# Performance work log

Hardware: AMD Instinct MI355X
Metric: run time of the kernel (lower is better)

## Reference

```python
import jax, jax.numpy as jnp
import numpy as np

E = 16      # num_experts
K = 4       # num_experts_per_tok
H = 2048    # hidden_size
I = 1408    # moe_intermediate_size
SI = 5632   # shared expert intermediate size
CAP = 1024
NORM_TOPK = False


def setup_inputs() -> dict:
    key = jax.random.key(0)
    ks = jax.random.split(key, 9)
    def w(k, shape, fan_in):
        return jax.random.normal(k, shape, jnp.float32) * (fan_in ** -0.5)
    return {
        "hidden_states": jax.random.normal(ks[0], (1, 2048, H), jnp.float32),
        "gate_w":  w(ks[1], (E, H), H),        # router: Linear(H -> E), no bias
        "we_gate": w(ks[2], (E, I, H), H),     # per-expert gate_proj weights
        "we_up":   w(ks[3], (E, I, H), H),     # per-expert up_proj weights
        "we_down": w(ks[4], (E, H, I), I),     # per-expert down_proj weights
        "ws_gate": w(ks[5], (SI, H), H),       # shared expert gate_proj
        "ws_up":   w(ks[6], (SI, H), H),       # shared expert up_proj
        "ws_down": w(ks[7], (H, SI), SI),      # shared expert down_proj
        "sg_w":    w(ks[8], (1, H), H),        # shared_expert_gate: Linear(H -> 1)
    }


def reference(hidden_states, gate_w, we_gate, we_up, we_down,
              ws_gate, ws_up, ws_down, sg_w):
    B, S, Hd = hidden_states.shape
    x = hidden_states.reshape(-1, Hd)                      # [T, H]
    T = x.shape[0]

    # --- router ---
    router_logits = x @ gate_w.T                           # [T, E]
    probs = jax.nn.softmax(router_logits.astype(jnp.float32), axis=-1)
    topw, topi = jax.lax.top_k(probs, K)                   # [T, K]
    if NORM_TOPK:
        topw = topw / topw.sum(axis=-1, keepdims=True)

    # --- dispatch: flatten (token, slot) assignments ---
    A = T * K
    fe = topi.reshape(A)                                   # expert id per assignment
    fw = topw.reshape(A)                                   # routing weight per assignment
    ft = jnp.repeat(jnp.arange(T), K)                      # token id per assignment
    # position of each assignment within its expert (rank in arrival order)
    oh = jax.nn.one_hot(fe, E, dtype=jnp.int32)            # [A, E]
    pos = jnp.take_along_axis(jnp.cumsum(oh, axis=0) - 1, fe[:, None], axis=1)[:, 0]
    valid = pos < CAP
    # scatter tokens into per-expert buffers; overflow goes to dummy row CAP
    buf = jnp.zeros((E, CAP + 1, Hd), x.dtype)
    buf = buf.at[fe, jnp.where(valid, pos, CAP)].set(x[ft])[:, :CAP]  # [E, C, H]

    # --- per-expert SiLU-gated MLP (batched grouped GEMMs) ---
    g = jnp.einsum('ech,eih->eci', buf, we_gate)
    u = jnp.einsum('ech,eih->eci', buf, we_up)
    eo = jnp.einsum('eci,ehi->ech', jax.nn.silu(g) * u, we_down)      # [E, C, H]

    # --- combine: weighted scatter-add back to tokens ---
    ga = eo[fe, jnp.minimum(pos, CAP - 1)]                 # [A, H]
    wcomb = (fw * valid.astype(fw.dtype)).astype(x.dtype)
    y = jnp.zeros((T, Hd), x.dtype).at[ft].add(ga * wcomb[:, None])

    # --- shared expert with sigmoid gate ---
    sh = (jax.nn.silu(x @ ws_gate.T) * (x @ ws_up.T)) @ ws_down.T
    sh = jax.nn.sigmoid(x @ sg_w.T) * sh

    out = (y + sh).reshape(B, S, Hd)
    return out, router_logits
```

## Files before the change

kernel.cpp:

```cpp
#include <hip/hip_runtime.h>

#define T_TOK 2048
#define NE 16
#define KTOP 4
#define HD 2048
#define ID 1408
#define SID 5632
#define CAPACITY 1024

typedef __attribute__((ext_vector_type(8))) short short8;
typedef __attribute__((ext_vector_type(4))) float floatx4;

__device__ __forceinline__ short f2b(float f){
  union { float f; unsigned u; } v; v.f = f;
  unsigned r = v.u + 0x7fffu + ((v.u >> 16) & 1u);
  return (short)(r >> 16);
}

__device__ __forceinline__ void gl16(const void* g, void* l){
  __builtin_amdgcn_global_load_lds(
      (const __attribute__((address_space(1))) void*)g,
      (__attribute__((address_space(3))) void*)l, 16, 0, 0);
}

__global__ void moe_zero(int* __restrict__ counts){
  if (threadIdx.x < NE) counts[threadIdx.x] = 0;
}

__global__ void moe_convert(const float* __restrict__ src, short* __restrict__ dst, int n8){
  int stride = gridDim.x * blockDim.x;
  for (int i = blockIdx.x * blockDim.x + threadIdx.x; i < n8; i += stride){
    float4 f0 = ((const float4*)src)[(size_t)i * 2];
    float4 f1 = ((const float4*)src)[(size_t)i * 2 + 1];
    short8 v = { f2b(f0.x), f2b(f0.y), f2b(f0.z), f2b(f0.w),
                 f2b(f1.x), f2b(f1.y), f2b(f1.z), f2b(f1.w) };
    ((short8*)dst)[i] = v;
  }
}

__global__ void moe_router(const float* __restrict__ x,
                           const float* __restrict__ gate_w,
                           const float* __restrict__ sg_w,
                           float* __restrict__ logits_out,
                           short* __restrict__ xb,
                           int* __restrict__ counts,
                           int* __restrict__ slot_token,
                           float* __restrict__ slot_w,
                           float* __restrict__ sg)
{
  int wave = threadIdx.x >> 6, lane = threadIdx.x & 63;
  int t = (blockIdx.x << 2) + wave;
  if (t >= T_TOK) return;
  const float4* xr = (const float4*)(x + (size_t)t * HD);
  short8* xbw = (short8*)(xb + (size_t)t * HD);
  float acc[17];
  #pragma unroll
  for (int e = 0; e < 17; ++e) acc[e] = 0.f;
  #pragma unroll
  for (int j = 0; j < 4; ++j){
    int i4 = (j * 64 + lane) * 2;
    float4 x0 = xr[i4], x1 = xr[i4 + 1];
    short8 v = { f2b(x0.x), f2b(x0.y), f2b(x0.z), f2b(x0.w),
                 f2b(x1.x), f2b(x1.y), f2b(x1.z), f2b(x1.w) };
    xbw[j * 64 + lane] = v;
    #pragma unroll
    for (int e = 0; e < 16; ++e){
      const float4* gr = (const float4*)(gate_w + e * HD);
      float4 g0 = gr[i4], g1 = gr[i4 + 1];
      acc[e] += x0.x*g0.x + x0.y*g0.y + x0.z*g0.z + x0.w*g0.w
              + x1.x*g1.x + x1.y*g1.y + x1.z*g1.z + x1.w*g1.w;
    }
    const float4* sr = (const float4*)sg_w;
    float4 s0 = sr[i4], s1 = sr[i4 + 1];
    acc[16] += x0.x*s0.x + x0.y*s0.y + x0.z*s0.z + x0.w*s0.w
             + x1.x*s1.x + x1.y*s1.y + x1.z*s1.z + x1.w*s1.w;
  }
  #pragma unroll
  for (int e = 0; e < 17; ++e){
    float v = acc[e];
    #pragma unroll
    for (int off = 32; off > 0; off >>= 1) v += __shfl_xor(v, off, 64);
    acc[e] = v;
  }
  if (lane == 0){
    float m = acc[0];
    #pragma unroll
    for (int e = 1; e < 16; ++e) m = fmaxf(m, acc[e]);
    float p[16]; float s = 0.f;
    #pragma unroll
    for (int e = 0; e < 16; ++e){ p[e] = expf(acc[e] - m); s += p[e]; }
    float inv = 1.f / s;
    #pragma unroll
    for (int e = 0; e < 16; ++e) logits_out[t * 16 + e] = acc[e];
    unsigned used = 0;
    for (int k = 0; k < KTOP; ++k){
      float best = -1.f; int bi = 0;
      #pragma unroll
      for (int e = 0; e < 16; ++e){
        float pe = ((used >> e) & 1u) ? -1.f : p[e];
        if (pe > best){ best = pe; bi = e; }
      }
      used |= (1u << bi);
      int pos = atomicAdd(&counts[bi], 1);
      if (pos < CAPACITY){
        slot_token[bi * CAPACITY + pos] = t;
        slot_w[bi * CAPACITY + pos] = best * inv;
      }
    }
    sg[t] = 1.f / (1.f + expf(-acc[16]));
  }
}


template<int BF16W>
__global__ __launch_bounds__(256) void moe_gateup(
    const short* __restrict__ Asrc,
    const void* __restrict__ Wg_, const void* __restrict__ Wu_,
    short* __restrict__ Out,
    const int* __restrict__ counts, const int* __restrict__ slot_token,
    int Ndim, int Kdim, int expert_mode, int mtiles, int ntiles)
{
  int nwg = gridDim.x;
  int wg = ((blockIdx.x & 7) * (nwg >> 3)) + (blockIdx.x >> 3);
  int m_t = wg % mtiles; wg /= mtiles;
  int n_t = wg % ntiles; int e = wg / ntiles;

  int cnt = T_TOK;
  size_t woff = 0;
  short* out = Out;
  if (expert_mode){
    cnt = counts[e]; if (cnt > CAPACITY) cnt = CAPACITY;
    if (m_t * 128 >= cnt) return;
    woff = (size_t)e * Ndim * Kdim;
    out = Out + (size_t)e * CAPACITY * Ndim;
  }
  const int m0 = m_t * 128, n0 = n_t * 64;

  __shared__ __align__(16) char smem[32768];
  char* sA  = smem;
  char* sBg = smem + 16384;
  char* sBu = smem + 24576;

  const int tid = threadIdx.x;
  const int lane = tid & 63, wave = tid >> 6;
  const int wr = wave >> 1, wc = wave & 1;
  const int lrow = lane & 15, lk = lane >> 4;

  const int srow  = tid >> 3;
  const int sxor  = srow & 7;
  const int pslot = tid & 7;
  const int lslot = pslot ^ sxor;

  const short* aptr[4];
  #pragma unroll
  for (int i = 0; i < 4; ++i){
    int p = m0 + i * 32 + srow;
    const short* base;
    if (expert_mode){
      int q = (p < cnt) ? p : 0;
      base = Asrc + (size_t)slot_token[e * CAPACITY + q] * Kdim;
    } else {
      base = Asrc + (size_t)p * Kdim;
    }
    aptr[i] = base + (lslot << 3);
  }
  const short *bgp[2], *bup[2];
  const float *bgf[2], *buf2[2];
  #pragma unroll
  for (int i = 0; i < 2; ++i){
    size_t roff = (size_t)(n0 + i * 32 + srow) * Kdim + (lslot << 3);
    if (BF16W){
      bgp[i] = (const short*)Wg_ + woff + roff;
      bup[i] = (const short*)Wu_ + woff + roff;
    } else {
      bgf[i]  = (const float*)Wg_ + woff + roff;
      buf2[i] = (const float*)Wu_ + woff + roff;
    }
  }

  const floatx4 vzero = {0.f, 0.f, 0.f, 0.f};
  floatx4 accg[4][2], accu[4][2];
  #pragma unroll
  for (int i = 0; i < 4; ++i)
    #pragma unroll
    for (int j = 0; j < 2; ++j){ accg[i][j] = vzero; accu[i][j] = vzero; }

  const int fxor = lrow & 7;
  const int arowb = (wr * 64 + lrow) << 7;
  const int browb = (wc * 32 + lrow) << 7;

  for (int k0 = 0; k0 < Kdim; k0 += 64){
    __syncthreads();
    if (BF16W){
      #pragma unroll
      for (int i = 0; i < 4; ++i) gl16(aptr[i] + k0, sA  + i * 4096 + tid * 16);
      #pragma unroll
      for (int i = 0; i < 2; ++i) gl16(bgp[i] + k0, sBg + i * 4096 + tid * 16);
      #pragma unroll
      for (int i = 0; i < 2; ++i) gl16(bup[i] + k0, sBu + i * 4096 + tid * 16);
    } else {
      #pragma unroll
      for (int i = 0; i < 4; ++i){
        short8 v = *(const short8*)(aptr[i] + k0);
        *(short8*)(sA + i * 4096 + tid * 16) = v;
      }
      #pragma unroll
      for (int i = 0; i < 2; ++i){
        float4 f0 = *(const float4*)(bgf[i] + k0);
        float4 f1 = *(const float4*)(bgf[i] + k0 + 4);
        short8 v = { f2b(f0.x), f2b(f0.y), f2b(f0.z), f2b(f0.w),
                     f2b(f1.x), f2b(f1.y), f2b(f1.z), f2b(f1.w) };
        *(short8*)(sBg + i * 4096 + tid * 16) = v;
        float4 g0 = *(const float4*)(buf2[i] + k0);
        float4 g1 = *(const float4*)(buf2[i] + k0 + 4);
        short8 w = { f2b(g0.x), f2b(g0.y), f2b(g0.z), f2b(g0.w),
                     f2b(g1.x), f2b(g1.y), f2b(g1.z), f2b(g1.w) };
        *(short8*)(sBu + i * 4096 + tid * 16) = w;
      }
    }
    __syncthreads();
    #pragma unroll
    for (int kh = 0; kh < 2; ++kh){
      const int soff = (((kh << 2) | lk) ^ fxor) << 4;
      short8 a[4], bg[2], bu[2];
      #pragma unroll
      for (int mf = 0; mf < 4; ++mf)
        a[mf] = *(const short8*)(sA + arowb + (mf << 11) + soff);
      #pragma unroll
      for (int nf = 0; nf < 2; ++nf){
        bg[nf] = *(const short8*)(sBg + browb + (nf << 11) + soff);
        bu[nf] = *(const short8*)(sBu + browb + (nf << 11) + soff);
      }
      #pragma unroll
      for (int mf = 0; mf < 4; ++mf)
        #pragma unroll
        for (int nf = 0; nf < 2; ++nf){
          accg[mf][nf] = __builtin_amdgcn_mfma_f32_16x16x32_bf16(a[mf], bg[nf], accg[mf][nf], 0, 0, 0);
          accu[mf][nf] = __builtin_amdgcn_mfma_f32_16x16x32_bf16(a[mf], bu[nf], accu[mf][nf], 0, 0, 0);
        }
    }
  }

  const int colbase = n0 + wc * 32 + lrow;
  #pragma unroll
  for (int mf = 0; mf < 4; ++mf){
    int pr = m0 + wr * 64 + mf * 16 + lk * 4;
    #pragma unroll
    for (int nf = 0; nf < 2; ++nf){
      floatx4 g4 = accg[mf][nf], u4 = accu[mf][nf];
      int col = colbase + nf * 16;
      #pragma unroll
      for (int r = 0; r < 4; ++r){
        float gv = g4[r], uv = u4[r];
        float a = (gv / (1.f + __expf(-gv))) * uv;
        out[(size_t)(pr + r) * Ndim + col] = f2b(a);
      }
    }
  }
}

template<int BF16W>
__global__ __launch_bounds__(256) void moe_down(
    const short* __restrict__ Asrc,
    const void* __restrict__ Wd_,
    float* __restrict__ y,
    const int* __restrict__ counts, const int* __restrict__ slot_token,
    const float* __restrict__ slot_w, const float* __restrict__ sgate,
    int Kdim, int expert_mode, int mtiles, int ntiles)
{
  int nwg = gridDim.x;
  int wg = ((blockIdx.x & 7) * (nwg >> 3)) + (blockIdx.x >> 3);
  int m_t = wg % mtiles; wg /= mtiles;
  int n_t = wg % ntiles; int e = wg / ntiles;

  int cnt = T_TOK;
  const short* ab = Asrc;
  size_t woff = 0;
  if (expert_mode){
    cnt = counts[e]; if (cnt > CAPACITY) cnt = CAPACITY;
    if (m_t * 128 >= cnt) return;
    ab = Asrc + (size_t)e * CAPACITY * Kdim;
    woff = (size_t)e * HD * Kdim;
  }
  const int m0 = m_t * 128, n0 = n_t * 128;

  __shared__ __align__(16) char smem[32768];
  char* sA = smem;
  char* sB = smem + 16384;

  const int tid = threadIdx.x;
  const int lane = tid & 63, wave = tid >> 6;
  const int wr = wave >> 1, wc = wave & 1;
  const int lrow = lane & 15, lk = lane >> 4;

  const int srow  = tid >> 3;
  const int sxor  = srow & 7;
  const int pslot = tid & 7;
  const int lslot = pslot ^ sxor;

  const short* aptr[4];
  const short* bbp[4];
  const float* bbf[4];
  #pragma unroll
  for (int i = 0; i < 4; ++i){
    aptr[i] = ab + (size_t)(m0 + i * 32 + srow) * Kdim + (lslot << 3);
    size_t roff = (size_t)(n0 + i * 32 + srow) * Kdim + (lslot << 3);
    if (BF16W) bbp[i] = (const short*)Wd_ + woff + roff;
    else       bbf[i] = (const float*)Wd_ + woff + roff;
  }

  const floatx4 vzero = {0.f, 0.f, 0.f, 0.f};
  floatx4 acc[4][4];
  #pragma unroll
  for (int i = 0; i < 4; ++i)
    #pragma unroll
    for (int j = 0; j < 4; ++j) acc[i][j] = vzero;

  const int fxor = lrow & 7;
  const int arowb = (wr * 64 + lrow) << 7;
  const int browb = (wc * 64 + lrow) << 7;

  for (int k0 = 0; k0 < Kdim; k0 += 64){
    __syncthreads();
    #pragma unroll
    for (int i = 0; i < 4; ++i){
      if (BF16W){
        gl16(aptr[i] + k0, sA + i * 4096 + tid * 16);
        gl16(bbp[i] + k0, sB + i * 4096 + tid * 16);
      } else {
        short8 v = *(const short8*)(aptr[i] + k0);
        *(short8*)(sA + i * 4096 + tid * 16) = v;
        float4 f0 = *(const float4*)(bbf[i] + k0);
        float4 f1 = *(const float4*)(bbf[i] + k0 + 4);
        short8 w = { f2b(f0.x), f2b(f0.y), f2b(f0.z), f2b(f0.w),
                     f2b(f1.x), f2b(f1.y), f2b(f1.z), f2b(f1.w) };
        *(short8*)(sB + i * 4096 + tid * 16) = w;
      }
    }
    __syncthreads();
    #pragma unroll
    for (int kh = 0; kh < 2; ++kh){
      const int soff = (((kh << 2) | lk) ^ fxor) << 4;
      short8 a[4], b[4];
      #pragma unroll
      for (int mf = 0; mf < 4; ++mf)
        a[mf] = *(const short8*)(sA + arowb + (mf << 11) + soff);
      #pragma unroll
      for (int nf = 0; nf < 4; ++nf)
        b[nf] = *(const short8*)(sB + browb + (nf << 11) + soff);
      #pragma unroll
      for (int mf = 0; mf < 4; ++mf)
        #pragma unroll
        for (int nf = 0; nf < 4; ++nf)
          acc[mf][nf] = __builtin_amdgcn_mfma_f32_16x16x32_bf16(a[mf], b[nf], acc[mf][nf], 0, 0, 0);
    }
  }

  const int colb = n0 + wc * 64 + lrow;
  if (expert_mode){
    #pragma unroll
    for (int mf = 0; mf < 4; ++mf){
      int pr = m0 + wr * 64 + mf * 16 + lk * 4;
      #pragma unroll
      for (int r = 0; r < 4; ++r){
        int p = pr + r;
        if (p < cnt){
          int tok = slot_token[e * CAPACITY + p];
          float w = slot_w[e * CAPACITY + p];
          #pragma unroll
          for (int nf = 0; nf < 4; ++nf)
            atomicAdd(&y[(size_t)tok * HD + colb + nf * 16], w * acc[mf][nf][r]);
        }
      }
    }
  } else {
    #pragma unroll
    for (int mf = 0; mf < 4; ++mf){
      int pr = m0 + wr * 64 + mf * 16 + lk * 4;
      #pragma unroll
      for (int r = 0; r < 4; ++r){
        int t = pr + r;
        float sv = sgate[t];
        #pragma unroll
        for (int nf = 0; nf < 4; ++nf)
          y[(size_t)t * HD + colb + nf * 16] = sv * acc[mf][nf][r];
      }
    }
  }
}

extern "C" void kernel_launch(void* const* d_in, const int* in_sizes, int n_in,
                              void* d_out, int out_size, void* d_ws, size_t ws_size,
                              hipStream_t stream)
{
  (void)in_sizes; (void)n_in; (void)out_size;
  const float* x       = (const float*)d_in[0];
  const float* gate_w  = (const float*)d_in[1];
  const float* we_gate = (const float*)d_in[2];
  const float* we_up   = (const float*)d_in[3];
  const float* we_down = (const float*)d_in[4];
  const float* wsg     = (const float*)d_in[5];
  const float* wsu     = (const float*)d_in[6];
  const float* wsd     = (const float*)d_in[7];
  const float* sg_w    = (const float*)d_in[8];

  float* y      = (float*)d_out;
  float* logits = y + (size_t)T_TOK * HD;

  const size_t SZ_XB  = (size_t)T_TOK * HD * 2;
  const size_t SZ_WE  = (size_t)NE * ID * HD * 2;
  const size_t SZ_WS  = (size_t)SID * HD * 2;
  const size_t SZ_ACT = (size_t)NE * CAPACITY * ID * 2;
  const size_t SZ_ACS = (size_t)T_TOK * SID * 2;

  char* ws = (char*)d_ws;

  size_t off = 0;
  short* xb   = (short*)(ws + off); off += SZ_XB;
  short* wbeg = (short*)(ws + off); off += SZ_WE;
  short* wbeu = (short*)(ws + off); off += SZ_WE;
  short* wbed = (short*)(ws + off); off += SZ_WE;
  short* wbsg = (short*)(ws + off); off += SZ_WS;
  short* wbsu = (short*)(ws + off); off += SZ_WS;
  short* wbsd = (short*)(ws + off); off += SZ_WS;
  short* act  = (short*)(ws + off); off += SZ_ACT;
  short* acts = (short*)(ws + off); off += SZ_ACS;
  int*   slot_token = (int*)  (ws + off); off += 65536;
  float* slot_w     = (float*)(ws + off); off += 65536;
  int*   counts     = (int*)  (ws + off); off += 256;
  float* sg         = (float*)(ws + off); off += 8192;
  const size_t WS_NEED = off;

  if (ws_size >= WS_NEED){
    moe_zero<<<1, 64, 0, stream>>>(counts);
    moe_convert<<<2048, 256, 0, stream>>>(we_gate, wbeg, NE * ID * HD / 8);
    moe_convert<<<2048, 256, 0, stream>>>(we_up,   wbeu, NE * ID * HD / 8);
    moe_convert<<<2048, 256, 0, stream>>>(we_down, wbed, NE * ID * HD / 8);
    moe_convert<<<2048, 256, 0, stream>>>(wsg, wbsg, SID * HD / 8);
    moe_convert<<<2048, 256, 0, stream>>>(wsu, wbsu, SID * HD / 8);
    moe_convert<<<2048, 256, 0, stream>>>(wsd, wbsd, SID * HD / 8);
    moe_router<<<512, 256, 0, stream>>>(x, gate_w, sg_w, logits, xb,
                                        counts, slot_token, slot_w, sg);
    moe_gateup<1><<<16 * 88, 256, 0, stream>>>(xb, wbsg, wbsu, acts,
                                               nullptr, nullptr, SID, HD, 0, 16, 88);
    moe_gateup<1><<<8 * 22 * NE, 256, 0, stream>>>(xb, wbeg, wbeu, act,
                                                   counts, slot_token, ID, HD, 1, 8, 22);
    moe_down<1><<<16 * 16, 256, 0, stream>>>(acts, wbsd, y, nullptr, nullptr,
                                             nullptr, sg, SID, 0, 16, 16);
    moe_down<1><<<8 * 16 * NE, 256, 0, stream>>>(act, wbed, y, counts, slot_token,
                                                 slot_w, nullptr, ID, 1, 8, 16);
  } else {
    size_t o2 = 0;
    short* xb2   = (short*)(ws + o2); o2 += SZ_XB;
    short* act2  = (short*)(ws + o2); o2 += SZ_ACT;
    short* acts2 = (short*)(ws + o2); o2 += SZ_ACS;
    int*   st2 = (int*)  (ws + o2); o2 += 65536;
    float* sw2 = (float*)(ws + o2); o2 += 65536;
    int*   cn2 = (int*)  (ws + o2); o2 += 256;
    float* sg2 = (float*)(ws + o2);
    moe_zero<<<1, 64, 0, stream>>>(cn2);
    moe_router<<<512, 256, 0, stream>>>(x, gate_w, sg_w, logits, xb2,
                                        cn2, st2, sw2, sg2);
    moe_gateup<0><<<16 * 88, 256, 0, stream>>>(xb2, wsg, wsu, acts2,
                                               nullptr, nullptr, SID, HD, 0, 16, 88);
    moe_gateup<0><<<8 * 22 * NE, 256, 0, stream>>>(xb2, we_gate, we_up, act2,
                                                   cn2, st2, ID, HD, 1, 8, 22);
    moe_down<0><<<16 * 16, 256, 0, stream>>>(acts2, wsd, y, nullptr, nullptr,
                                             nullptr, sg2, SID, 0, 16, 16);
    moe_down<0><<<8 * 16 * NE, 256, 0, stream>>>(act2, we_down, y, cn2, st2,
                                                 sw2, nullptr, ID, 1, 8, 16);
  }
}
```

Baseline: 913.3 us.

## Double-buffer GEMM LDS, fuse weight conversions, replace atomic combine with gather kernel

Merges the six weight-conversion launches into one kernel. Adds double-buffered LDS prefetch to the bf16 gate/up and down GEMM loops so global-to-LDS loads for the next K tile overlap the MFMA work on the current one. Halves the shared-expert down N-tile to launch more workgroups. When workspace allows, expert outputs are written as bf16 to a buffer and a per-token combine kernel gathers them, replacing float atomicAdd scatter. This costs extra memory traffic, doubled LDS use per block, and bf16 rounding of expert outputs before combine.

Result: faster. 841.6 us (-7.9%).

```diff
diff --git a/kernel.cpp b/kernel.cpp
--- a/kernel.cpp
+++ b/kernel.cpp
@@ -16,7 +16,10 @@
   unsigned r = v.u + 0x7fffu + ((v.u >> 16) & 1u);
   return (short)(r >> 16);
 }
-
+__device__ __forceinline__ float b2f(short s){
+  union { float f; unsigned u; } v; v.u = ((unsigned)(unsigned short)s) << 16;
+  return v.f;
+}
 __device__ __forceinline__ void gl16(const void* g, void* l){
   __builtin_amdgcn_global_load_lds(
       (const __attribute__((address_space(1))) void*)g,
@@ -27,11 +30,25 @@
   if (threadIdx.x < NE) counts[threadIdx.x] = 0;
 }
 
-__global__ void moe_convert(const float* __restrict__ src, short* __restrict__ dst, int n8){
-  int stride = gridDim.x * blockDim.x;
-  for (int i = blockIdx.x * blockDim.x + threadIdx.x; i < n8; i += stride){
-    float4 f0 = ((const float4*)src)[(size_t)i * 2];
-    float4 f1 = ((const float4*)src)[(size_t)i * 2 + 1];
+__global__ void moe_convert_all(const float* __restrict__ eg, const float* __restrict__ eu,
+                                const float* __restrict__ ed, const float* __restrict__ sgp,
+                                const float* __restrict__ sup, const float* __restrict__ sdp,
+                                short* __restrict__ dst)
+{
+  const long long EW = (long long)NE * ID * HD / 8;
+  const long long SW = (long long)SID * HD / 8;
+  const long long total = 3 * EW + 3 * SW;
+  long long stride = (long long)gridDim.x * blockDim.x;
+  for (long long i = (long long)blockIdx.x * blockDim.x + threadIdx.x; i < total; i += stride){
+    const float* s; long long j;
+    if (i < 2 * EW){
+      if (i < EW){ s = eg; j = i; } else { s = eu; j = i - EW; }
+    } else if (i < 3 * EW){ s = ed; j = i - 2 * EW; }
+    else if (i < 3 * EW + SW){ s = sgp; j = i - 3 * EW; }
+    else if (i < 3 * EW + 2 * SW){ s = sup; j = i - 3 * EW - SW; }
+    else { s = sdp; j = i - 3 * EW - 2 * SW; }
+    float4 f0 = ((const float4*)s)[j * 2];
+    float4 f1 = ((const float4*)s)[j * 2 + 1];
     short8 v = { f2b(f0.x), f2b(f0.y), f2b(f0.z), f2b(f0.w),
                  f2b(f1.x), f2b(f1.y), f2b(f1.z), f2b(f1.w) };
     ((short8*)dst)[i] = v;
@@ -46,6 +63,8 @@
                            int* __restrict__ counts,
                            int* __restrict__ slot_token,
                            float* __restrict__ slot_w,
+                           int* __restrict__ tslot,
+                           float* __restrict__ tw,
                            float* __restrict__ sg)
 {
   int wave = threadIdx.x >> 6, lane = threadIdx.x & 63;
@@ -102,10 +121,14 @@
       }
       used |= (1u << bi);
       int pos = atomicAdd(&counts[bi], 1);
+      int enc = -1;
       if (pos < CAPACITY){
         slot_token[bi * CAPACITY + pos] = t;
         slot_w[bi * CAPACITY + pos] = best * inv;
-      }
+        enc = bi * CAPACITY + pos;
+      }
+      tslot[t * KTOP + k] = enc;
+      tw[t * KTOP + k] = best * inv;
     }
     sg[t] = 1.f / (1.f + expf(-acc[16]));
   }
@@ -125,9 +148,7 @@
   int m_t = wg % mtiles; wg /= mtiles;
   int n_t = wg % ntiles; int e = wg / ntiles;
 
-  int cnt = T_TOK;
-  size_t woff = 0;
-  short* out = Out;
+  int cnt = T_TOK; size_t woff = 0; short* out = Out;
   if (expert_mode){
     cnt = counts[e]; if (cnt > CAPACITY) cnt = CAPACITY;
     if (m_t * 128 >= cnt) return;
@@ -136,20 +157,15 @@
   }
   const int m0 = m_t * 128, n0 = n_t * 64;
 
-  __shared__ __align__(16) char smem[32768];
-  char* sA  = smem;
-  char* sBg = smem + 16384;
-  char* sBu = smem + 24576;
+  __shared__ __align__(16) char smem[2][32768];
 
   const int tid = threadIdx.x;
   const int lane = tid & 63, wave = tid >> 6;
   const int wr = wave >> 1, wc = wave & 1;
   const int lrow = lane & 15, lk = lane >> 4;
 
-  const int srow  = tid >> 3;
-  const int sxor  = srow & 7;
-  const int pslot = tid & 7;
-  const int lslot = pslot ^ sxor;
+  const int srow = tid >> 3, pslot = tid & 7;
+  const int lslot = pslot ^ (srow & 7);
 
   const short* aptr[4];
   #pragma unroll
@@ -159,9 +175,7 @@
     if (expert_mode){
       int q = (p < cnt) ? p : 0;
       base = Asrc + (size_t)slot_token[e * CAPACITY + q] * Kdim;
-    } else {
-      base = Asrc + (size_t)p * Kdim;
-    }
+    } else base = Asrc + (size_t)p * Kdim;
     aptr[i] = base + (lslot << 3);
   }
   const short *bgp[2], *bup[2];
@@ -189,16 +203,56 @@
   const int arowb = (wr * 64 + lrow) << 7;
   const int browb = (wc * 32 + lrow) << 7;
 
-  for (int k0 = 0; k0 < Kdim; k0 += 64){
+  if (BF16W){
+    {
+      char* b = smem[0];
+      #pragma unroll
+      for (int i = 0; i < 4; ++i) gl16(aptr[i], b + i * 4096 + tid * 16);
+      #pragma unroll
+      for (int i = 0; i < 2; ++i) gl16(bgp[i], b + 16384 + i * 4096 + tid * 16);
+      #pragma unroll
+      for (int i = 0; i < 2; ++i) gl16(bup[i], b + 24576 + i * 4096 + tid * 16);
+    }
     __syncthreads();
-    if (BF16W){
-      #pragma unroll
-      for (int i = 0; i < 4; ++i) gl16(aptr[i] + k0, sA  + i * 4096 + tid * 16);
-      #pragma unroll
-      for (int i = 0; i < 2; ++i) gl16(bgp[i] + k0, sBg + i * 4096 + tid * 16);
-      #pragma unroll
-      for (int i = 0; i < 2; ++i) gl16(bup[i] + k0, sBu + i * 4096 + tid * 16);
-    } else {
+    int cur = 0;
+    for (int k0 = 0; k0 < Kdim; k0 += 64){
+      if (k0 + 64 < Kdim){
+        char* b = smem[cur ^ 1];
+        #pragma unroll
+        for (int i = 0; i < 4; ++i) gl16(aptr[i] + k0 + 64, b + i * 4096 + tid * 16);
+        #pragma unroll
+        for (int i = 0; i < 2; ++i) gl16(bgp[i] + k0 + 64, b + 16384 + i * 4096 + tid * 16);
+        #pragma unroll
+        for (int i = 0; i < 2; ++i) gl16(bup[i] + k0 + 64, b + 24576 + i * 4096 + tid * 16);
+      }
+      const char* bb = smem[cur];
+      #pragma unroll
+      for (int kh = 0; kh < 2; ++kh){
+        const int soff = (((kh << 2) | lk) ^ fxor) << 4;
+        short8 a[4], bg[2], bu[2];
+        #pragma unroll
+        for (int mf = 0; mf < 4; ++mf)
+          a[mf] = *(const short8*)(bb + arowb + (mf << 11) + soff);
+        #pragma unroll
+        for (int nf = 0; nf < 2; ++nf){
+          bg[nf] = *(const short8*)(bb + 16384 + browb + (nf << 11) + soff);
+          bu[nf] = *(const short8*)(bb + 24576 + browb + (nf << 11) + soff);
+        }
+        #pragma unroll
+        for (int mf = 0; mf < 4; ++mf)
+          #pragma unroll
+          for (int nf = 0; nf < 2; ++nf){
+            accg[mf][nf] = __builtin_amdgcn_mfma_f32_16x16x32_bf16(a[mf], bg[nf], accg[mf][nf], 0, 0, 0);
+            accu[mf][nf] = __builtin_amdgcn_mfma_f32_16x16x32_bf16(a[mf], bu[nf], accu[mf][nf], 0, 0, 0);
+          }
+      }
+      __syncthreads();
+      cur ^= 1;
+    }
+  } else {
+    char* sA = smem[0]; char* sBg = sA + 16384; char* sBu = sA + 24576;
+    for (int k0 = 0; k0 < Kdim; k0 += 64){
+      __syncthreads();
       #pragma unroll
       for (int i = 0; i < 4; ++i){
         short8 v = *(const short8*)(aptr[i] + k0);
@@ -217,27 +271,27 @@
                      f2b(g1.x), f2b(g1.y), f2b(g1.z), f2b(g1.w) };
         *(short8*)(sBu + i * 4096 + tid * 16) = w;
       }
-    }
-    __syncthreads();
-    #pragma unroll
-    for (int kh = 0; kh < 2; ++kh){
-      const int soff = (((kh << 2) | lk) ^ fxor) << 4;
-      short8 a[4], bg[2], bu[2];
-      #pragma unroll
-      for (int mf = 0; mf < 4; ++mf)
-        a[mf] = *(const short8*)(sA + arowb + (mf << 11) + soff);
-      #pragma unroll
-      for (int nf = 0; nf < 2; ++nf){
-        bg[nf] = *(const short8*)(sBg + browb + (nf << 11) + soff);
-        bu[nf] = *(const short8*)(sBu + browb + (nf << 11) + soff);
-      }
-      #pragma unroll
-      for (int mf = 0; mf < 4; ++mf)
+      __syncthreads();
+      #pragma unroll
+      for (int kh = 0; kh < 2; ++kh){
+        const int soff = (((kh << 2) | lk) ^ fxor) << 4;
+        short8 a[4], bg[2], bu[2];
+        #pragma unroll
+        for (int mf = 0; mf < 4; ++mf)
+          a[mf] = *(const short8*)(sA + arowb + (mf << 11) + soff);
         #pragma unroll
         for (int nf = 0; nf < 2; ++nf){
-          accg[mf][nf] = __builtin_amdgcn_mfma_f32_16x16x32_bf16(a[mf], bg[nf], accg[mf][nf], 0, 0, 0);
-          accu[mf][nf] = __builtin_amdgcn_mfma_f32_16x16x32_bf16(a[mf], bu[nf], accu[mf][nf], 0, 0, 0);
+          bg[nf] = *(const short8*)(sBg + browb + (nf << 11) + soff);
+          bu[nf] = *(const short8*)(sBu + browb + (nf << 11) + soff);
         }
+        #pragma unroll
+        for (int mf = 0; mf < 4; ++mf)
+          #pragma unroll
+          for (int nf = 0; nf < 2; ++nf){
+            accg[mf][nf] = __builtin_amdgcn_mfma_f32_16x16x32_bf16(a[mf], bg[nf], accg[mf][nf], 0, 0, 0);
+            accu[mf][nf] = __builtin_amdgcn_mfma_f32_16x16x32_bf16(a[mf], bu[nf], accu[mf][nf], 0, 0, 0);
+          }
+      }
     }
   }
 
@@ -259,117 +313,166 @@
   }
 }
 
-template<int BF16W>
+template<int BF16W, int NF>
 __global__ __launch_bounds__(256) void moe_down(
-    const short* __restrict__ Asrc,
-    const void* __restrict__ Wd_,
-    float* __restrict__ y,
+    const short* __restrict__ Asrc, const void* __restrict__ Wd_,
+    float* __restrict__ y, short* __restrict__ eo,
     const int* __restrict__ counts, const int* __restrict__ slot_token,
     const float* __restrict__ slot_w, const float* __restrict__ sgate,
     int Kdim, int expert_mode, int mtiles, int ntiles)
 {
+  constexpr int BN = NF * 32;
   int nwg = gridDim.x;
   int wg = ((blockIdx.x & 7) * (nwg >> 3)) + (blockIdx.x >> 3);
   int m_t = wg % mtiles; wg /= mtiles;
   int n_t = wg % ntiles; int e = wg / ntiles;
 
-  int cnt = T_TOK;
-  const short* ab = Asrc;
-  size_t woff = 0;
+  int cnt = T_TOK; const short* ab = Asrc; size_t woff = 0;
   if (expert_mode){
     cnt = counts[e]; if (cnt > CAPACITY) cnt = CAPACITY;
     if (m_t * 128 >= cnt) return;
     ab = Asrc + (size_t)e * CAPACITY * Kdim;
     woff = (size_t)e * HD * Kdim;
   }
-  const int m0 = m_t * 128, n0 = n_t * 128;
-
-  __shared__ __align__(16) char smem[32768];
-  char* sA = smem;
-  char* sB = smem + 16384;
+  const int m0 = m_t * 128, n0 = n_t * BN;
+
+  __shared__ __align__(16) char smem[2][16384 + NF * 4096];
 
   const int tid = threadIdx.x;
   const int lane = tid & 63, wave = tid >> 6;
   const int wr = wave >> 1, wc = wave & 1;
   const int lrow = lane & 15, lk = lane >> 4;
 
-  const int srow  = tid >> 3;
-  const int sxor  = srow & 7;
-  const int pslot = tid & 7;
-  const int lslot = pslot ^ sxor;
+  const int srow = tid >> 3, pslot = tid & 7;
+  const int lslot = pslot ^ (srow & 7);
 
   const short* aptr[4];
-  const short* bbp[4];
-  const float* bbf[4];
-  #pragma unroll
-  for (int i = 0; i < 4; ++i){
+  #pragma unroll
+  for (int i = 0; i < 4; ++i)
     aptr[i] = ab + (size_t)(m0 + i * 32 + srow) * Kdim + (lslot << 3);
+  const short* bbp[NF];
+  const float* bbf[NF];
+  #pragma unroll
+  for (int i = 0; i < NF; ++i){
     size_t roff = (size_t)(n0 + i * 32 + srow) * Kdim + (lslot << 3);
     if (BF16W) bbp[i] = (const short*)Wd_ + woff + roff;
     else       bbf[i] = (const float*)Wd_ + woff + roff;
   }
 
   const floatx4 vzero = {0.f, 0.f, 0.f, 0.f};
-  floatx4 acc[4][4];
+  floatx4 acc[4][NF];
   #pragma unroll
   for (int i = 0; i < 4; ++i)
     #pragma unroll
-    for (int j = 0; j < 4; ++j) acc[i][j] = vzero;
+    for (int j = 0; j < NF; ++j) acc[i][j] = vzero;
 
   const int fxor = lrow & 7;
   const int arowb = (wr * 64 + lrow) << 7;
-  const int browb = (wc * 64 + lrow) << 7;
-
-  for (int k0 = 0; k0 < Kdim; k0 += 64){
+  const int browb = (wc * (NF * 16) + lrow) << 7;
+
+  if (BF16W){
+    {
+      char* b = smem[0];
+      #pragma unroll
+      for (int i = 0; i < 4; ++i) gl16(aptr[i], b + i * 4096 + tid * 16);
+      #pragma unroll
+      for (int i = 0; i < NF; ++i) gl16(bbp[i], b + 16384 + i * 4096 + tid * 16);
+    }
     __syncthreads();
-    #pragma unroll
-    for (int i = 0; i < 4; ++i){
-      if (BF16W){
-        gl16(aptr[i] + k0, sA + i * 4096 + tid * 16);
-        gl16(bbp[i] + k0, sB + i * 4096 + tid * 16);
-      } else {
+    int cur = 0;
+    for (int k0 = 0; k0 < Kdim; k0 += 64){
+      if (k0 + 64 < Kdim){
+        char* b = smem[cur ^ 1];
+        #pragma unroll
+        for (int i = 0; i < 4; ++i) gl16(aptr[i] + k0 + 64, b + i * 4096 + tid * 16);
+        #pragma unroll
+        for (int i = 0; i < NF; ++i) gl16(bbp[i] + k0 + 64, b + 16384 + i * 4096 + tid * 16);
+      }
+      const char* bb = smem[cur];
+      #pragma unroll
+      for (int kh = 0; kh < 2; ++kh){
+        const int soff = (((kh << 2) | lk) ^ fxor) << 4;
+        short8 a[4], b[NF];
+        #pragma unroll
+        for (int mf = 0; mf < 4; ++mf)
+          a[mf] = *(const short8*)(bb + arowb + (mf << 11) + soff);
+        #pragma unroll
+        for (int nf = 0; nf < NF; ++nf)
+          b[nf] = *(const short8*)(bb + 16384 + browb + (nf << 11) + soff);
+        #pragma unroll
+        for (int mf = 0; mf < 4; ++mf)
+          #pragma unroll
+          for (int nf = 0; nf < NF; ++nf)
+            acc[mf][nf] = __builtin_amdgcn_mfma_f32_16x16x32_bf16(a[mf], b[nf], acc[mf][nf], 0, 0, 0);
+      }
+      __syncthreads();
+      cur ^= 1;
+    }
+  } else {
+    char* sA = smem[0]; char* sB = sA + 16384;
+    for (int k0 = 0; k0 < Kdim; k0 += 64){
+      __syncthreads();
+      #pragma unroll
+      for (int i = 0; i < 4; ++i){
         short8 v = *(const short8*)(aptr[i] + k0);
         *(short8*)(sA + i * 4096 + tid * 16) = v;
+      }
+      #pragma unroll
+      for (int i = 0; i < NF; ++i){
         float4 f0 = *(const float4*)(bbf[i] + k0);
         float4 f1 = *(const float4*)(bbf[i] + k0 + 4);
         short8 w = { f2b(f0.x), f2b(f0.y), f2b(f0.z), f2b(f0.w),
                      f2b(f1.x), f2b(f1.y), f2b(f1.z), f2b(f1.w) };
         *(short8*)(sB + i * 4096 + tid * 16) = w;
       }
-    }
-    __syncthreads();
-    #pragma unroll
-    for (int kh = 0; kh < 2; ++kh){
-      const int soff = (((kh << 2) | lk) ^ fxor) << 4;
-      short8 a[4], b[4];
-      #pragma unroll
-      for (int mf = 0; mf < 4; ++mf)
-        a[mf] = *(const short8*)(sA + arowb + (mf << 11) + soff);
-      #pragma unroll
-      for (int nf = 0; nf < 4; ++nf)
-        b[nf] = *(const short8*)(sB + browb + (nf << 11) + soff);
-      #pragma unroll
-      for (int mf = 0; mf < 4; ++mf)
-        #pragma unroll
-        for (int nf = 0; nf < 4; ++nf)
-          acc[mf][nf] = __builtin_amdgcn_mfma_f32_16x16x32_bf16(a[mf], b[nf], acc[mf][nf], 0, 0, 0);
-    }
-  }
-
-  const int colb = n0 + wc * 64 + lrow;
+      __syncthreads();
+      #pragma unroll
+      for (int kh = 0; kh < 2; ++kh){
+        const int soff = (((kh << 2) | lk) ^ fxor) << 4;
+        short8 a[4], b[NF];
+        #pragma unroll
+        for (int mf = 0; mf < 4; ++mf)
+          a[mf] = *(const short8*)(sA + arowb + (mf << 11) + soff);
+        #pragma unroll
+        for (int nf = 0; nf < NF; ++nf)
+          b[nf] = *(const short8*)(sB + browb + (nf << 11) + soff);
+        #pragma unroll
+        for (int mf = 0; mf < 4; ++mf)
+          #pragma unroll
+          for (int nf = 0; nf < NF; ++nf)
+            acc[mf][nf] = __builtin_amdgcn_mfma_f32_16x16x32_bf16(a[mf], b[nf], acc[mf][nf], 0, 0, 0);
+      }
+    }
+  }
+
+  const int colb = n0 + wc * (NF * 16) + lrow;
   if (expert_mode){
-    #pragma unroll
-    for (int mf = 0; mf < 4; ++mf){
-      int pr = m0 + wr * 64 + mf * 16 + lk * 4;
-      #pragma unroll
-      for (int r = 0; r < 4; ++r){
-        int p = pr + r;
-        if (p < cnt){
-          int tok = slot_token[e * CAPACITY + p];
-          float w = slot_w[e * CAPACITY + p];
+    if (eo){
+      #pragma unroll
+      for (int mf = 0; mf < 4; ++mf){
+        int pr = m0 + wr * 64 + mf * 16 + lk * 4;
+        #pragma unroll
+        for (int r = 0; r < 4; ++r){
+          int p = pr + r;
           #pragma unroll
-          for (int nf = 0; nf < 4; ++nf)
-            atomicAdd(&y[(size_t)tok * HD + colb + nf * 16], w * acc[mf][nf][r]);
+          for (int nf = 0; nf < NF; ++nf)
+            eo[(size_t)(e * CAPACITY + p) * HD + colb + nf * 16] = f2b(acc[mf][nf][r]);
+        }
+      }
+    } else {
+      #pragma unroll
+      for (int mf = 0; mf < 4; ++mf){
+        int pr = m0 + wr * 64 + mf * 16 + lk * 4;
+        #pragma unroll
+        for (int r = 0; r < 4; ++r){
+          int p = pr + r;
+          if (p < cnt){
+            int tok = slot_token[e * CAPACITY + p];
+            float w = slot_w[e * CAPACITY + p];
+            #pragma unroll
+            for (int nf = 0; nf < NF; ++nf)
+              atomicAdd(&y[(size_t)tok * HD + colb + nf * 16], w * acc[mf][nf][r]);
+          }
         }
       }
     }
@@ -382,11 +485,36 @@
         int t = pr + r;
         float sv = sgate[t];
         #pragma unroll
-        for (int nf = 0; nf < 4; ++nf)
+        for (int nf = 0; nf < NF; ++nf)
           y[(size_t)t * HD + colb + nf * 16] = sv * acc[mf][nf][r];
       }
     }
   }
+}
+
+__global__ void moe_combine(const short* __restrict__ eo,
+                            const int* __restrict__ tslot,
+                            const float* __restrict__ tw,
+                            float* __restrict__ y)
+{
+  int t = blockIdx.x;
+  int o = threadIdx.x << 3;
+  float* yp = y + (size_t)t * HD + o;
+  float4 a0 = *(const float4*)yp, a1 = *(const float4*)(yp + 4);
+  float acc[8] = {a0.x, a0.y, a0.z, a0.w, a1.x, a1.y, a1.z, a1.w};
+  #pragma unroll
+  for (int k = 0; k < KTOP; ++k){
+    int s = tslot[t * KTOP + k];
+    if (s >= 0){
+      float w = tw[t * KTOP + k];
+      short8 v = *(const short8*)(eo + (size_t)s * HD + o);
+      #pragma unroll
+      for (int j = 0; j < 8; ++j) acc[j] += w * b2f(v[j]);
+    }
+  }
+  float4 r0 = {acc[0], acc[1], acc[2], acc[3]};
+  float4 r1 = {acc[4], acc[5], acc[6], acc[7]};
+  *(float4*)yp = r0; *(float4*)(yp + 4) = r1;
 }
 
 extern "C" void kernel_launch(void* const* d_in, const int* in_sizes, int n_in,
@@ -412,9 +540,13 @@
   const size_t SZ_WS  = (size_t)SID * HD * 2;
   const size_t SZ_ACT = (size_t)NE * CAPACITY * ID * 2;
   const size_t SZ_ACS = (size_t)T_TOK * SID * 2;
+  const size_t SZ_EO  = (size_t)NE * CAPACITY * HD * 2;
+  const size_t SZ_SMALL = 65536 + 65536 + 32768 + 32768 + 256 + 8192;
+
+  const size_t NEED_B = SZ_XB + 3 * SZ_WE + 3 * SZ_WS + SZ_ACT + SZ_ACS + SZ_SMALL;
+  const size_t NEED_A = NEED_B + SZ_EO;
 
   char* ws = (char*)d_ws;
-
   size_t off = 0;
   short* xb   = (short*)(ws + off); off += SZ_XB;
   short* wbeg = (short*)(ws + off); off += SZ_WE;
@@ -425,30 +557,29 @@
   short* wbsd = (short*)(ws + off); off += SZ_WS;
   short* act  = (short*)(ws + off); off += SZ_ACT;
   short* acts = (short*)(ws + off); off += SZ_ACS;
+  short* eo   = (short*)(ws + off);
+  if (ws_size >= NEED_A) off += SZ_EO; else eo = nullptr;
   int*   slot_token = (int*)  (ws + off); off += 65536;
   float* slot_w     = (float*)(ws + off); off += 65536;
+  int*   tslot      = (int*)  (ws + off); off += 32768;
+  float* tw         = (float*)(ws + off); off += 32768;
   int*   counts     = (int*)  (ws + off); off += 256;
-  float* sg         = (float*)(ws + off); off += 8192;
-  const size_t WS_NEED = off;
-
-  if (ws_size >= WS_NEED){
+  float* sg         = (float*)(ws + off);
+
+  if (ws_size >= NEED_B){
     moe_zero<<<1, 64, 0, stream>>>(counts);
-    moe_convert<<<2048, 256, 0, stream>>>(we_gate, wbeg, NE * ID * HD / 8);
-    moe_convert<<<2048, 256, 0, stream>>>(we_up,   wbeu, NE * ID * HD / 8);
-    moe_convert<<<2048, 256, 0, stream>>>(we_down, wbed, NE * ID * HD / 8);
-    moe_convert<<<2048, 256, 0, stream>>>(wsg, wbsg, SID * HD / 8);
-    moe_convert<<<2048, 256, 0, stream>>>(wsu, wbsu, SID * HD / 8);
-    moe_convert<<<2048, 256, 0, stream>>>(wsd, wbsd, SID * HD / 8);
+    moe_convert_all<<<2048, 256, 0, stream>>>(we_gate, we_up, we_down, wsg, wsu, wsd, wbeg);
     moe_router<<<512, 256, 0, stream>>>(x, gate_w, sg_w, logits, xb,
-                                        counts, slot_token, slot_w, sg);
+                                        counts, slot_token, slot_w, tslot, tw, sg);
     moe_gateup<1><<<16 * 88, 256, 0, stream>>>(xb, wbsg, wbsu, acts,
                                                nullptr, nullptr, SID, HD, 0, 16, 88);
     moe_gateup<1><<<8 * 22 * NE, 256, 0, stream>>>(xb, wbeg, wbeu, act,
                                                    counts, slot_token, ID, HD, 1, 8, 22);
-    moe_down<1><<<16 * 16, 256, 0, stream>>>(acts, wbsd, y, nullptr, nullptr,
-                                             nullptr, sg, SID, 0, 16, 16);
-    moe_down<1><<<8 * 16 * NE, 256, 0, stream>>>(act, wbed, y, counts, slot_token,
-                                                 slot_w, nullptr, ID, 1, 8, 16);
+    moe_down<1, 2><<<16 * 32, 256, 0, stream>>>(acts, wbsd, y, nullptr, nullptr, nullptr,
+                                                nullptr, sg, SID, 0, 16, 32);
+    moe_down<1, 4><<<8 * 16 * NE, 256, 0, stream>>>(act, wbed, y, eo, counts, slot_token,
+                                                    slot_w, nullptr, ID, 1, 8, 16);
+    if (eo) moe_combine<<<T_TOK, 256, 0, stream>>>(eo, tslot, tw, y);
   } else {
     size_t o2 = 0;
     short* xb2   = (short*)(ws + o2); o2 += SZ_XB;
@@ -456,18 +587,20 @@
     short* acts2 = (short*)(ws + o2); o2 += SZ_ACS;
     int*   st2 = (int*)  (ws + o2); o2 += 65536;
     float* sw2 = (float*)(ws + o2); o2 += 65536;
+    int*   ts2 = (int*)  (ws + o2); o2 += 32768;
+    float* tw2 = (float*)(ws + o2); o2 += 32768;
     int*   cn2 = (int*)  (ws + o2); o2 += 256;
     float* sg2 = (float*)(ws + o2);
     moe_zero<<<1, 64, 0, stream>>>(cn2);
     moe_router<<<512, 256, 0, stream>>>(x, gate_w, sg_w, logits, xb2,
-                                        cn2, st2, sw2, sg2);
+                                        cn2, st2, sw2, ts2, tw2, sg2);
     moe_gateup<0><<<16 * 88, 256, 0, stream>>>(xb2, wsg, wsu, acts2,
                                                nullptr, nullptr, SID, HD, 0, 16, 88);
     moe_gateup<0><<<8 * 22 * NE, 256, 0, stream>>>(xb2, we_gate, we_up, act2,
                                                    cn2, st2, ID, HD, 1, 8, 22);
-    moe_down<0><<<16 * 16, 256, 0, stream>>>(acts2, wsd, y, nullptr, nullptr,
-                                             nullptr, sg2, SID, 0, 16, 16);
-    moe_down<0><<<8 * 16 * NE, 256, 0, stream>>>(act2, we_down, y, cn2, st2,
-                                                 sw2, nullptr, ID, 1, 8, 16);
-  }
-}
+    moe_down<0, 2><<<16 * 32, 256, 0, stream>>>(acts2, wsd, y, nullptr, nullptr, nullptr,
+                                                nullptr, sg2, SID, 0, 16, 32);
+    moe_down<0, 4><<<8 * 16 * NE, 256, 0, stream>>>(act2, we_down, y, nullptr, cn2, st2,
+                                                    sw2, nullptr, ID, 1, 8, 16);
+  }
+}
```
